# Optimization experiments

Measured on AMD Instinct MI355X. Metric: run time of the kernel, lower is better.

## Reference

```python
import jax, jax.numpy as jnp
import numpy as np

D_MODEL = 1024
NUM_HEADS = 16
HEAD_DIM = D_MODEL // NUM_HEADS
B, S = 2, 2048


def setup_inputs() -> dict:
    key = jax.random.key(0)
    ks = jax.random.split(key, 8)
    scale = 1.0 / np.sqrt(D_MODEL)
    inp = {
        "query": jax.random.normal(ks[0], (B, S, D_MODEL), jnp.float32),
        "key": jax.random.normal(ks[1], (B, S, D_MODEL), jnp.float32),
        "value": jax.random.normal(ks[2], (B, S, D_MODEL), jnp.float32),
        # causal mask, broadcastable over batch and heads
        "mask": jnp.tril(jnp.ones((S, S), dtype=bool))[None, None, :, :],
        # torch nn.Linear weights: y = x @ W.T (+ b)
        "Wq": jax.random.normal(ks[3], (D_MODEL, D_MODEL), jnp.float32) * scale,
        "Wk": jax.random.normal(ks[4], (D_MODEL, D_MODEL), jnp.float32) * scale,
        "Wv": jax.random.normal(ks[5], (D_MODEL, D_MODEL), jnp.float32) * scale,
        "Wo": jax.random.normal(ks[6], (D_MODEL, D_MODEL), jnp.float32) * scale,
        "bo": jax.random.normal(ks[7], (D_MODEL,), jnp.float32) * scale,
    }
    return inp


def _split_heads(x):
    b, s, _ = x.shape
    return x.reshape(b, s, NUM_HEADS, HEAD_DIM).transpose(0, 2, 1, 3)  # [B,H,S,Dh]


def reference(query, key, value, mask, Wq, Wk, Wv, Wo, bo):
    q = _split_heads(query @ Wq.T)
    k = _split_heads(key @ Wk.T)
    v = _split_heads(value @ Wv.T)
    scores = jnp.einsum("bhqd,bhkd->bhqk", q, k) / jnp.sqrt(jnp.float32(HEAD_DIM))
    scores = jnp.where(mask, scores, jnp.float32(-jnp.inf))
    attn = jax.nn.softmax(scores, axis=-1)
    out = jnp.einsum("bhqk,bhkd->bhqd", attn, v)  # [B,H,S,Dh]
    out = out.transpose(0, 2, 1, 3).reshape(query.shape[0], q.shape[2], D_MODEL)
    return out @ Wo.T + bo
```

## Files before the change

kernel.cpp:

```cpp
#include <hip/hip_runtime.h>
#include <hip/hip_bf16.h>

#define DM   1024
#define NH   16
#define HD   64
#define SEQ  2048
#define BATCH 2
#define MTOT (BATCH*SEQ)

typedef unsigned short u16;
typedef __attribute__((ext_vector_type(8))) short bf16x8;
typedef __attribute__((ext_vector_type(4))) float f32x4;

#define SC2F 0.1803368801111464f

__device__ __forceinline__ float bf2f(u16 h) {
  union { unsigned int i; float f; } u; u.i = ((unsigned int)h) << 16; return u.f;
}
__device__ __forceinline__ u16 f2bf(float f) {
  union { float f; unsigned int i; } u; u.f = f;
  unsigned int r = u.i + 0x7fffu + ((u.i >> 16) & 1u);
  return (u16)(r >> 16);
}
__device__ __forceinline__ unsigned int pk2(float lo, float hi) {
  union { float f; unsigned int u; } a, b; a.f = lo; b.f = hi;
  return ((a.u + 0x8000u) >> 16) | ((b.u + 0x8000u) & 0xFFFF0000u);
}
__device__ __forceinline__ unsigned int cvtpk(float lo, float hi) {
  unsigned int r;
  asm("v_cvt_pk_bf16_f32 %0, %1, %2" : "=v"(r) : "v"(lo), "v"(hi));
  return r;
}

__device__ __forceinline__ uint4 load8_bf16(const void* base, size_t elemOff, bool isf32) {
  if (!isf32) return *(const uint4*)((const u16*)base + elemOff);
  const float* f = (const float*)base + elemOff;
  f32x4 a = *(const f32x4*)f;
  f32x4 b = *(const f32x4*)(f + 4);
  union { u16 h[8]; uint4 v; } r;
  r.h[0]=f2bf(a[0]); r.h[1]=f2bf(a[1]); r.h[2]=f2bf(a[2]); r.h[3]=f2bf(a[3]);
  r.h[4]=f2bf(b[0]); r.h[5]=f2bf(b[1]); r.h[6]=f2bf(b[2]); r.h[7]=f2bf(b[3]);
  return r.v;
}

__global__ __launch_bounds__(256) void prep(
    const void* __restrict__ q, const void* __restrict__ k, const void* __restrict__ v,
    const void* __restrict__ wq, const void* __restrict__ wk, const void* __restrict__ wv,
    const void* __restrict__ wo, const void* __restrict__ bo,
    u16* __restrict__ Xq, u16* __restrict__ Xk, u16* __restrict__ Xv,
    u16* __restrict__ Wqb, u16* __restrict__ Wkb, u16* __restrict__ Wvb, u16* __restrict__ Wob,
    float* __restrict__ biasf, int* __restrict__ flag_out)
{
  const int tid = threadIdx.x;
  __shared__ int cnts[4];
  {
    const u16* qs = (const u16*)q;
    int e0 = (qs[tid*2]   >> 7) & 0xFF;
    int e1 = (qs[tid*2+1] >> 7) & 0xFF;
    int c = ((e0 >= 0x6E && e0 <= 0x8F) ? 1 : 0) + ((e1 >= 0x6E && e1 <= 0x8F) ? 1 : 0);
    c += __shfl_xor(c, 1);  c += __shfl_xor(c, 2);  c += __shfl_xor(c, 4);
    c += __shfl_xor(c, 8);  c += __shfl_xor(c, 16); c += __shfl_xor(c, 32);
    if ((tid & 63) == 0) cnts[tid >> 6] = c;
  }
  __syncthreads();
  const bool isf32 = (cnts[0] + cnts[1] + cnts[2] + cnts[3]) < 400;

  const int z = blockIdx.z;
  if (z == 7) {
    if (blockIdx.x == 0) {
      if (tid == 0) *flag_out = isf32 ? 0 : 1;
      for (int i = tid; i < DM; i += 256)
        biasf[i] = isf32 ? ((const float*)bo)[i] : bf2f(((const u16*)bo)[i]);
    }
    return;
  }
  const void* src; u16* dst; size_t n;
  switch (z) {
    case 0: src=q;  dst=Xq;  n=(size_t)MTOT*DM; break;
    case 1: src=k;  dst=Xk;  n=(size_t)MTOT*DM; break;
    case 2: src=v;  dst=Xv;  n=(size_t)MTOT*DM; break;
    case 3: src=wq; dst=Wqb; n=(size_t)DM*DM;   break;
    case 4: src=wk; dst=Wkb; n=(size_t)DM*DM;   break;
    case 5: src=wv; dst=Wvb; n=(size_t)DM*DM;   break;
    default: src=wo; dst=Wob; n=(size_t)DM*DM;  break;
  }
  const size_t stride = (size_t)gridDim.x * 256 * 8;
  for (size_t i = ((size_t)blockIdx.x * 256 + tid) * 8; i < n; i += stride)
    *(uint4*)(dst + i) = load8_bf16(src, i, isf32);
}

__device__ __forceinline__ void gld16(const u16* g, u16* l) {
  __builtin_amdgcn_global_load_lds(
      (const __attribute__((address_space(1))) void*)g,
      (__attribute__((address_space(3))) void*)l, 16, 0, 0);
}

__global__ __launch_bounds__(256) void gemm_qkv(
    const u16* __restrict__ X0, const u16* __restrict__ X1, const u16* __restrict__ X2,
    const u16* __restrict__ W0, const u16* __restrict__ W1, const u16* __restrict__ W2,
    u16* __restrict__ F0, u16* __restrict__ F1, u16* __restrict__ F2)
{
  __shared__ __align__(16) u16 smem[24576];
  u16* const A0 = smem;
  u16* const A1 = smem + 4096;
  u16* const A2 = smem + 8192;
  u16* const B0 = smem + 12288;
  u16* const B1 = smem + 16384;
  u16* const B2 = smem + 20480;

  const int zz = blockIdx.z;
  const u16* X = (zz==0) ? X0 : ((zz==1) ? X1 : X2);
  const u16* W = (zz==0) ? W0 : ((zz==1) ? W1 : W2);
  u16* outF    = (zz==0) ? F0 : ((zz==1) ? F1 : F2);

  const int tid = threadIdx.x;
  const int wave = tid >> 6, lane = tid & 63, quad = lane >> 4, l16 = lane & 15;
  const int wr = wave >> 1, wc = wave & 1;
  const int m0 = blockIdx.x * 128, n0 = blockIdx.y * 128;

  const int sg = ((lane & 3) ^ ((lane >> 3) & 3)) * 8;
  const int rS = wave*32 + (lane >> 2);
  const u16* gA0 = X + (size_t)(m0 + rS)*DM + sg;
  const u16* gA1 = X + (size_t)(m0 + rS + 16)*DM + sg;
  const u16* gB0 = W + (size_t)(n0 + rS)*DM + sg;
  const u16* gB1 = W + (size_t)(n0 + rS + 16)*DM + sg;
  const int so = wave*1024;

  const int xslot8 = (quad ^ ((l16 >> 1) & 3)) * 8;

  f32x4 acc[4][4];
#pragma unroll
  for (int i = 0; i < 4; i++)
#pragma unroll
    for (int j = 0; j < 4; j++) { acc[i][j][0]=0.f; acc[i][j][1]=0.f; acc[i][j][2]=0.f; acc[i][j][3]=0.f; }

  gld16(gA0, A0 + so);
  gld16(gA1, A0 + so + 512);
  gld16(gB0, B0 + so);
  gld16(gB1, B0 + so + 512);
  asm volatile("" ::: "memory");

  int cur = 0;
  for (int k0 = 0; k0 < DM; k0 += 32) {
    u16* const Ab = (cur == 0) ? A0 : ((cur == 1) ? A1 : A2);
    u16* const Bb = (cur == 0) ? B0 : ((cur == 1) ? B1 : B2);
    const int nxt = (cur == 2) ? 0 : cur + 1;
    if (k0 + 32 < DM) {
      u16* const An = (nxt == 0) ? A0 : ((nxt == 1) ? A1 : A2);
      u16* const Bn = (nxt == 0) ? B0 : ((nxt == 1) ? B1 : B2);
      gld16(gA0 + k0 + 32, An + so);
      gld16(gA1 + k0 + 32, An + so + 512);
      gld16(gB0 + k0 + 32, Bn + so);
      gld16(gB1 + k0 + 32, Bn + so + 512);
      asm volatile("s_waitcnt vmcnt(4)" ::: "memory");
    } else {
      asm volatile("s_waitcnt vmcnt(0)" ::: "memory");
    }
    __builtin_amdgcn_s_barrier();
    asm volatile("" ::: "memory");

    bf16x8 af[4], bfr[4];
#pragma unroll
    for (int fr = 0; fr < 4; fr++)
      af[fr] = *(const bf16x8*)&Ab[(wr*64 + fr*16 + l16)*32 + xslot8];
#pragma unroll
    for (int fc = 0; fc < 4; fc++)
      bfr[fc] = *(const bf16x8*)&Bb[(wc*64 + fc*16 + l16)*32 + xslot8];
#pragma unroll
    for (int fr = 0; fr < 4; fr++)
#pragma unroll
      for (int fc = 0; fc < 4; fc++)
        acc[fr][fc] = __builtin_amdgcn_mfma_f32_16x16x32_bf16(af[fr], bfr[fc], acc[fr][fc], 0, 0, 0);

    asm volatile("" ::: "memory");
    cur = nxt;
  }

  if (zz == 2) {
    u16* const Ts = smem;
    const int bb = m0 >> 11;
    const int s0 = m0 & (SEQ-1);
#pragma unroll
    for (int p = 0; p < 2; p++) {
      __syncthreads();
      if (wc == p) {
#pragma unroll
        for (int fr = 0; fr < 4; fr++) {
#pragma unroll
          for (int fc = 0; fc < 4; fc++) {
            const int dl = fc*16 + l16;
            const int sb = wr*64 + fr*16 + quad*4;
            const int slot = (sb >> 3) ^ (dl & 15);
            u16* rowp = &Ts[dl*128 + slot*8 + (sb & 7)];
            *(unsigned int*)(rowp)     = pk2(acc[fr][fc][0], acc[fr][fc][1]);
            *(unsigned int*)(rowp + 2) = pk2(acc[fr][fc][2], acc[fr][fc][3]);
          }
        }
      }
      __syncthreads();
      const int dl2 = tid >> 2, ch4 = tid & 3;
      const int hh = (n0 + p*64) >> 6;
      u16* dst = outF + ((size_t)(bb*NH + hh)*HD + dl2)*SEQ + s0 + ch4*32;
#pragma unroll
      for (int j = 0; j < 4; j++) {
        const int c  = ch4*4 + j;
        const int lo = (c >> 2)*32 + (c & 3)*4;
        const int hi = lo + 16;
        uint2 lo2 = *(const uint2*)&Ts[dl2*128 + (((lo >> 3) ^ (dl2 & 15))*8) + (lo & 7)];
        uint2 hi2 = *(const uint2*)&Ts[dl2*128 + (((hi >> 3) ^ (dl2 & 15))*8) + (hi & 7)];
        uint4 o; o.x = lo2.x; o.y = lo2.y; o.z = hi2.x; o.w = hi2.y;
        *(uint4*)&dst[j*8] = o;
      }
    }
    return;
  }

#pragma unroll
  for (int fr = 0; fr < 4; fr++) {
#pragma unroll
    for (int rr = 0; rr < 4; rr++) {
      const int m = m0 + wr*64 + fr*16 + quad*4 + rr;
#pragma unroll
      for (int fc = 0; fc < 4; fc++) {
        const int n = n0 + wc*64 + fc*16 + l16;
        float vv = acc[fr][fc][rr];
        if (zz == 0) vv *= SC2F;
        const int b = m >> 11, s = m & (SEQ-1), h = n >> 6, d = n & (HD-1);
        outF[((size_t)(b*NH + h)*SEQ + s)*HD + d] = f2bf(vv);
      }
    }
  }
}

__global__ __launch_bounds__(256) void gemm_out(
    const u16* __restrict__ X, const u16* __restrict__ W,
    const float* __restrict__ biasf, void* __restrict__ outP,
    const int* __restrict__ dflag)
{
  __shared__ __align__(16) u16 smem[18432];
  u16* const A0 = smem;
  u16* const A1 = smem + 4096;
  u16* const A2 = smem + 8192;
  u16* const B0 = smem + 12288;
  u16* const B1 = smem + 14336;
  u16* const B2 = smem + 16384;

  const int tid = threadIdx.x;
  const int wave = tid >> 6, lane = tid & 63, quad = lane >> 4, l16 = lane & 15;
  const int wr = wave >> 1, wc = wave & 1;
  const int m0 = blockIdx.x * 128, n0 = blockIdx.y * 64;

  const int sg = ((lane & 3) ^ ((lane >> 3) & 3)) * 8;
  const int rA = wave*32 + (lane >> 2);
  const int rB = wave*16 + (lane >> 2);
  const u16* gA0 = X + (size_t)(m0 + rA)*DM + sg;
  const u16* gA1 = X + (size_t)(m0 + rA + 16)*DM + sg;
  const u16* gB0 = W + (size_t)(n0 + rB)*DM + sg;
  const int soA = wave*1024, soB = wave*512;

  const int xslot8 = (quad ^ ((l16 >> 1) & 3)) * 8;

  f32x4 acc[4][2];
#pragma unroll
  for (int i = 0; i < 4; i++)
#pragma unroll
    for (int j = 0; j < 2; j++) { acc[i][j][0]=0.f; acc[i][j][1]=0.f; acc[i][j][2]=0.f; acc[i][j][3]=0.f; }

  gld16(gA0, A0 + soA);
  gld16(gA1, A0 + soA + 512);
  gld16(gB0, B0 + soB);
  asm volatile("" ::: "memory");

  int cur = 0;
  for (int k0 = 0; k0 < DM; k0 += 32) {
    u16* const Ab = (cur == 0) ? A0 : ((cur == 1) ? A1 : A2);
    u16* const Bb = (cur == 0) ? B0 : ((cur == 1) ? B1 : B2);
    const int nxt = (cur == 2) ? 0 : cur + 1;
    if (k0 + 32 < DM) {
      u16* const An = (nxt == 0) ? A0 : ((nxt == 1) ? A1 : A2);
      u16* const Bn = (nxt == 0) ? B0 : ((nxt == 1) ? B1 : B2);
      gld16(gA0 + k0 + 32, An + soA);
      gld16(gA1 + k0 + 32, An + soA + 512);
      gld16(gB0 + k0 + 32, Bn + soB);
      asm volatile("s_waitcnt vmcnt(3)" ::: "memory");
    } else {
      asm volatile("s_waitcnt vmcnt(0)" ::: "memory");
    }
    __builtin_amdgcn_s_barrier();
    asm volatile("" ::: "memory");

    bf16x8 af[4], bfr[2];
#pragma unroll
    for (int fr = 0; fr < 4; fr++)
      af[fr] = *(const bf16x8*)&Ab[(wr*64 + fr*16 + l16)*32 + xslot8];
#pragma unroll
    for (int fc = 0; fc < 2; fc++)
      bfr[fc] = *(const bf16x8*)&Bb[(wc*32 + fc*16 + l16)*32 + xslot8];
#pragma unroll
    for (int fr = 0; fr < 4; fr++)
#pragma unroll
      for (int fc = 0; fc < 2; fc++)
        acc[fr][fc] = __builtin_amdgcn_mfma_f32_16x16x32_bf16(af[fr], bfr[fc], acc[fr][fc], 0, 0, 0);

    asm volatile("" ::: "memory");
    cur = nxt;
  }

  const bool isf32 = (*dflag == 0);
#pragma unroll
  for (int fr = 0; fr < 4; fr++) {
#pragma unroll
    for (int rr = 0; rr < 4; rr++) {
      const int m = m0 + wr*64 + fr*16 + quad*4 + rr;
#pragma unroll
      for (int fc = 0; fc < 2; fc++) {
        const int n = n0 + wc*32 + fc*16 + l16;
        float vv = acc[fr][fc][rr] + biasf[n];
        if (isf32) ((float*)outP)[(size_t)m*DM + n] = vv;
        else       ((u16*)outP)[(size_t)m*DM + n]   = f2bf(vv);
      }
    }
  }
}

__global__ __launch_bounds__(256) void attn_mfma(
    const u16* __restrict__ Qb, const u16* __restrict__ Kb,
    const u16* __restrict__ Vtb,
    u16* __restrict__ Opart, float* __restrict__ mlpart)
{
  __shared__ u16 Ks[2][64*64];
  __shared__ u16 Vs[2][64*64];

  const int bh = blockIdx.x;
  const int pr = blockIdx.y, z = blockIdx.z;
  const u16* Qp = Qb  + (size_t)bh * SEQ * HD;
  const u16* Kp = Kb  + (size_t)bh * SEQ * HD;
  const u16* Vp = Vtb + (size_t)bh * HD * SEQ;

  const int tid  = threadIdx.x;
  const int wave = tid >> 6, lane = tid & 63, quad = lane >> 4, l16 = lane & 15;

  const int i0 = wave*128 + lane, i1 = i0 + 64;
  const int r0 = i0 >> 3, c0 = (i0 & 7) ^ (r0 & 7);
  const int r1 = i1 >> 3, c1 = (i1 & 7) ^ (r1 & 7);
  const int kq_off0 = r0*HD + c0*8;
  const int kq_off1 = r1*HD + c1*8;
  const int v_off0  = r0*SEQ + c0*8;
  const int v_off1  = r1*SEQ + c1*8;

  const int l7 = l16 & 7;
  const int ql = wave*16 + l16;
  const int so = wave*1024;

  for (int ph = 0; ph < 2; ph++) {
    const int qt = ph ? (31 - pr) : pr;
    const int n = qt + 1, half = (n + 1) >> 1;
    const int klo = z ? half : 0, khi = z ? n : half;
    const int q0 = qt * 64;
    const int qg = q0 + ql;

    const u16* qrow = Qp + (size_t)qg * HD;
    const bf16x8 bq0 = *(const bf16x8*)(qrow + quad*8);
    const bf16x8 bq1 = *(const bf16x8*)(qrow + 32 + quad*8);

    f32x4 O[4];
#pragma unroll
    for (int u = 0; u < 4; u++) { O[u][0]=0.f; O[u][1]=0.f; O[u][2]=0.f; O[u][3]=0.f; }
    float mi = -__builtin_inff();
    f32x4 lv = {0.f, 0.f, 0.f, 0.f};

    if (klo < khi) {
      gld16(Kp + klo*(64*HD) + kq_off0, &Ks[0][so]);
      gld16(Kp + klo*(64*HD) + kq_off1, &Ks[0][so + 512]);
      gld16(Vp + klo*64 + v_off0, &Vs[0][so]);
      gld16(Vp + klo*64 + v_off1, &Vs[0][so + 512]);
    }
    asm volatile("" ::: "memory");

    for (int kt = klo; kt < khi; kt++) {
      const int cb = (kt - klo) & 1;
      const u16* kb = &Ks[cb][0];
      const u16* vb = &Vs[cb][0];
      if (kt + 1 < khi) {
        u16* kn = &Ks[cb ^ 1][so];
        u16* vn = &Vs[cb ^ 1][so];
        gld16(Kp + (kt+1)*(64*HD) + kq_off0, kn);
        gld16(Kp + (kt+1)*(64*HD) + kq_off1, kn + 512);
        gld16(Vp + (kt+1)*64 + v_off0, vn);
        gld16(Vp + (kt+1)*64 + v_off1, vn + 512);
        asm volatile("s_waitcnt vmcnt(4)" ::: "memory");
      } else {
        asm volatile("s_waitcnt vmcnt(0)" ::: "memory");
      }
      __builtin_amdgcn_s_barrier();
      asm volatile("" ::: "memory");

      f32x4 st[4];
#pragma unroll
      for (int t = 0; t < 4; t++) { st[t][0]=0.f; st[t][1]=0.f; st[t][2]=0.f; st[t][3]=0.f; }
#pragma unroll
      for (int s = 0; s < 2; s++) {
        const bf16x8 bq = s ? bq1 : bq0;
        const int ch = s*4 + quad;
#pragma unroll
        for (int t = 0; t < 4; t++) {
          bf16x8 ak = *(const bf16x8*)&kb[((t*16 + l16)*8 + (ch ^ l7))*8];
          st[t] = __builtin_amdgcn_mfma_f32_16x16x32_bf16(ak, bq, st[t], 0, 0, 0);
        }
      }

      if (kt == qt) {
#pragma unroll
        for (int t = 0; t < 4; t++)
#pragma unroll
          for (int r = 0; r < 4; r++)
            if (kt*64 + t*16 + quad*4 + r > qg) st[t][r] = -__builtin_inff();
      }

      f32x4 m01 = __builtin_elementwise_max(st[0], st[1]);
      f32x4 m23 = __builtin_elementwise_max(st[2], st[3]);
      f32x4 mm  = __builtin_elementwise_max(m01, m23);
      float mx = fmaxf(fmaxf(mm[0], mm[1]), fmaxf(mm[2], mm[3]));
      mx = fmaxf(mx, __shfl_xor(mx, 16));
      mx = fmaxf(mx, __shfl_xor(mx, 32));

      if (__any(mx > mi + 8.0f)) {
        const float nm = fmaxf(mi, mx);
        const float al = exp2f(mi - nm);
        mi = nm;
        const f32x4 alv = {al, al, al, al};
        lv *= alv;
        O[0] *= alv; O[1] *= alv; O[2] *= alv; O[3] *= alv;
      }

      const f32x4 miv = {mi, mi, mi, mi};
      unsigned int w[4][2];
      f32x4 e0, e1, e2, e3;
      {
        f32x4 d0 = st[0] - miv, d1 = st[1] - miv, d2 = st[2] - miv, d3 = st[3] - miv;
        e0[0]=exp2f(d0[0]); e0[1]=exp2f(d0[1]); e0[2]=exp2f(d0[2]); e0[3]=exp2f(d0[3]);
        e1[0]=exp2f(d1[0]); e1[1]=exp2f(d1[1]); e1[2]=exp2f(d1[2]); e1[3]=exp2f(d1[3]);
        e2[0]=exp2f(d2[0]); e2[1]=exp2f(d2[1]); e2[2]=exp2f(d2[2]); e2[3]=exp2f(d2[3]);
        e3[0]=exp2f(d3[0]); e3[1]=exp2f(d3[1]); e3[2]=exp2f(d3[2]); e3[3]=exp2f(d3[3]);
      }
      w[0][0] = cvtpk(e0[0], e0[1]); w[0][1] = cvtpk(e0[2], e0[3]);
      w[1][0] = cvtpk(e1[0], e1[1]); w[1][1] = cvtpk(e1[2], e1[3]);
      w[2][0] = cvtpk(e2[0], e2[1]); w[2][1] = cvtpk(e2[2], e2[3]);
      w[3][0] = cvtpk(e3[0], e3[1]); w[3][1] = cvtpk(e3[2], e3[3]);
      lv += (e0 + e1) + (e2 + e3);

#pragma unroll
      for (int s = 0; s < 2; s++) {
        union { unsigned int u[4]; bf16x8 v; } bp;
        bp.u[0] = w[2*s][0];   bp.u[1] = w[2*s][1];
        bp.u[2] = w[2*s+1][0]; bp.u[3] = w[2*s+1][1];
        const int ch = s*4 + quad;
#pragma unroll
        for (int u = 0; u < 4; u++) {
          bf16x8 av = *(const bf16x8*)&vb[((u*16 + l16)*8 + (ch ^ l7))*8];
          O[u] = __builtin_amdgcn_mfma_f32_16x16x32_bf16(av, bp.v, O[u], 0, 0, 0);
        }
      }

      asm volatile("" ::: "memory");
      __builtin_amdgcn_s_barrier();
      asm volatile("" ::: "memory");
    }

    float ls = (lv[0] + lv[1]) + (lv[2] + lv[3]);
    ls += __shfl_xor(ls, 16);
    ls += __shfl_xor(ls, 32);

    const int pi = (bh*32 + qt)*2 + z;
    u16* op = Opart + (size_t)pi*4096 + ql*64;
#pragma unroll
    for (int u = 0; u < 4; u++) {
      uint2 u2; u2.x = pk2(O[u][0], O[u][1]); u2.y = pk2(O[u][2], O[u][3]);
      *(uint2*)&op[u*16 + quad*4] = u2;
    }
    if (quad == 0) {
      float2 ml2; ml2.x = mi; ml2.y = ls;
      *(float2*)&mlpart[(size_t)pi*128 + ql*2] = ml2;
    }
  }
}

__global__ __launch_bounds__(64) void attn_merge(
    const u16* __restrict__ Opart, const float* __restrict__ mlpart,
    u16* __restrict__ aO)
{
  const int g = blockIdx.x;
  const int bh = g & 31, qt = g >> 5;
  const int b = bh >> 4, h = bh & 15;
  const int t = threadIdx.x;
  const int pi0 = (bh*32 + qt)*2, pi1 = pi0 + 1;

  const float2 ml0 = *(const float2*)&mlpart[(size_t)pi0*128 + t*2];
  const float2 ml1 = *(const float2*)&mlpart[(size_t)pi1*128 + t*2];
  const float M = fmaxf(ml0.x, ml1.x);
  float w0 = exp2f(ml0.x - M), w1 = exp2f(ml1.x - M);
  const float inv = 1.0f / (w0*ml0.y + w1*ml1.y);
  w0 *= inv; w1 *= inv;

  const u16* o0 = Opart + (size_t)pi0*4096 + t*64;
  const u16* o1 = Opart + (size_t)pi1*4096 + t*64;
  u16* out = aO + (size_t)(b*SEQ + qt*64 + t)*DM + h*HD;
#pragma unroll
  for (int d0 = 0; d0 < 64; d0 += 8) {
    union { uint4 v; u16 h[8]; } a, c; union { uint4 v; u16 h[8]; } bb;
    a.v  = *(const uint4*)&o0[d0];
    bb.v = *(const uint4*)&o1[d0];
#pragma unroll
    for (int j = 0; j < 8; j += 2) {
      float x0 = w0*bf2f(a.h[j])   + w1*bf2f(bb.h[j]);
      float x1 = w0*bf2f(a.h[j+1]) + w1*bf2f(bb.h[j+1]);
      unsigned int pk = pk2(x0, x1);
      c.h[j] = (u16)(pk & 0xFFFF); c.h[j+1] = (u16)(pk >> 16);
    }
    *(uint4*)&out[d0] = c.v;
  }
}

extern "C" void kernel_launch(void* const* d_in, const int* in_sizes, int n_in,
                              void* d_out, int out_size, void* d_ws, size_t ws_size,
                              hipStream_t stream) {
  const void* q  = d_in[0];
  const void* k  = d_in[1];
  const void* v  = d_in[2];
  const void* wq = d_in[4];
  const void* wk = d_in[5];
  const void* wv = d_in[6];
  const void* wo = d_in[7];
  const void* bo = d_in[8];

  const size_t TX = (size_t)MTOT*DM;
  const size_t TW = (size_t)DM*DM;
  u16* ws  = (u16*)d_ws;
  u16* Xq  = ws;
  u16* Xk  = ws + TX;
  u16* Xv  = ws + 2*TX;
  u16* Wqb = ws + 3*TX;
  u16* Wkb = Wqb + TW;
  u16* Wvb = Wqb + 2*TW;
  u16* Wob = Wqb + 3*TW;
  u16* Qw  = ws + 3*TX + 4*TW;
  u16* Kw  = Qw + TX;
  u16* Vt  = Qw + 2*TX;
  u16*   Opart  = Xk;
  float* mlpart = (float*)Wqb;
  u16*   aO     = Xq;
  float* biasf  = (float*)(Qw + 3*TX);
  int*   fl     = (int*)(biasf + DM);

  dim3 blk(256);
  prep<<<dim3(512, 1, 8), blk, 0, stream>>>(q, k, v, wq, wk, wv, wo, bo,
      Xq, Xk, Xv, Wqb, Wkb, Wvb, Wob, biasf, fl);
  gemm_qkv<<<dim3(MTOT/128, DM/128, 3), blk, 0, stream>>>(
      Xq, Xk, Xv, Wqb, Wkb, Wvb, Qw, Kw, Vt);
  attn_mfma<<<dim3(BATCH*NH, 16, 2), blk, 0, stream>>>(Qw, Kw, Vt, Opart, mlpart);
  attn_merge<<<dim3(32*32), dim3(64), 0, stream>>>(Opart, mlpart, aO);
  gemm_out<<<dim3(MTOT/128, DM/64), blk, 0, stream>>>(aO, Wob, biasf, d_out, fl);
}
```

Baseline: 230.3 us.

## Drop split-K attention and merge kernel; one block per query tile

Replaces the split-KV attention (two partial halves per query tile plus a separate merge kernel) with one block per query tile that walks the full causal key range and normalizes its output directly. Query tiles are mapped to blocks in an interleaved long/short order to balance causal work. This removes the merge launch and the round trip of partial outputs and statistics through global memory. In exchange each block is serial over up to 32 key tiles with only 1024 blocks, so load imbalance and the critical path may grow.

```diff
diff --git a/kernel.cpp b/kernel.cpp
--- a/kernel.cpp
+++ b/kernel.cpp
@@ -326,13 +326,19 @@
 __global__ __launch_bounds__(256) void attn_mfma(
     const u16* __restrict__ Qb, const u16* __restrict__ Kb,
     const u16* __restrict__ Vtb,
-    u16* __restrict__ Opart, float* __restrict__ mlpart)
+    u16* __restrict__ aO)
 {
   __shared__ u16 Ks[2][64*64];
   __shared__ u16 Vs[2][64*64];
 
   const int bh = blockIdx.x;
-  const int pr = blockIdx.y, z = blockIdx.z;
+  const int py = blockIdx.y;
+  int qt;
+  if      (py < 8)  qt = 31 - py;
+  else if (py < 16) qt = py - 8;
+  else if (py < 24) qt = 39 - py;
+  else              qt = py - 16;
+
   const u16* Qp = Qb  + (size_t)bh * SEQ * HD;
   const u16* Kp = Kb  + (size_t)bh * SEQ * HD;
   const u16* Vp = Vtb + (size_t)bh * HD * SEQ;
@@ -352,172 +358,128 @@
   const int ql = wave*16 + l16;
   const int so = wave*1024;
 
-  for (int ph = 0; ph < 2; ph++) {
-    const int qt = ph ? (31 - pr) : pr;
-    const int n = qt + 1, half = (n + 1) >> 1;
-    const int klo = z ? half : 0, khi = z ? n : half;
-    const int q0 = qt * 64;
-    const int qg = q0 + ql;
-
-    const u16* qrow = Qp + (size_t)qg * HD;
-    const bf16x8 bq0 = *(const bf16x8*)(qrow + quad*8);
-    const bf16x8 bq1 = *(const bf16x8*)(qrow + 32 + quad*8);
-
-    f32x4 O[4];
-#pragma unroll
-    for (int u = 0; u < 4; u++) { O[u][0]=0.f; O[u][1]=0.f; O[u][2]=0.f; O[u][3]=0.f; }
-    float mi = -__builtin_inff();
-    f32x4 lv = {0.f, 0.f, 0.f, 0.f};
-
-    if (klo < khi) {
-      gld16(Kp + klo*(64*HD) + kq_off0, &Ks[0][so]);
-      gld16(Kp + klo*(64*HD) + kq_off1, &Ks[0][so + 512]);
-      gld16(Vp + klo*64 + v_off0, &Vs[0][so]);
-      gld16(Vp + klo*64 + v_off1, &Vs[0][so + 512]);
-    }
-    asm volatile("" ::: "memory");
-
-    for (int kt = klo; kt < khi; kt++) {
-      const int cb = (kt - klo) & 1;
-      const u16* kb = &Ks[cb][0];
-      const u16* vb = &Vs[cb][0];
-      if (kt + 1 < khi) {
-        u16* kn = &Ks[cb ^ 1][so];
-        u16* vn = &Vs[cb ^ 1][so];
-        gld16(Kp + (kt+1)*(64*HD) + kq_off0, kn);
-        gld16(Kp + (kt+1)*(64*HD) + kq_off1, kn + 512);
-        gld16(Vp + (kt+1)*64 + v_off0, vn);
-        gld16(Vp + (kt+1)*64 + v_off1, vn + 512);
-        asm volatile("s_waitcnt vmcnt(4)" ::: "memory");
-      } else {
-        asm volatile("s_waitcnt vmcnt(0)" ::: "memory");
+  const int khi = qt + 1;
+  const int qg = qt*64 + ql;
+
+  const u16* qrow = Qp + (size_t)qg * HD;
+  const bf16x8 bq0 = *(const bf16x8*)(qrow + quad*8);
+  const bf16x8 bq1 = *(const bf16x8*)(qrow + 32 + quad*8);
+
+  f32x4 O[4];
+#pragma unroll
+  for (int u = 0; u < 4; u++) { O[u][0]=0.f; O[u][1]=0.f; O[u][2]=0.f; O[u][3]=0.f; }
+  float mi = -__builtin_inff();
+  f32x4 lv = {0.f, 0.f, 0.f, 0.f};
+
+  gld16(Kp + kq_off0, &Ks[0][so]);
+  gld16(Kp + kq_off1, &Ks[0][so + 512]);
+  gld16(Vp + v_off0, &Vs[0][so]);
+  gld16(Vp + v_off1, &Vs[0][so + 512]);
+  asm volatile("" ::: "memory");
+
+  for (int kt = 0; kt < khi; kt++) {
+    const int cb = kt & 1;
+    const u16* kb = &Ks[cb][0];
+    const u16* vb = &Vs[cb][0];
+    if (kt + 1 < khi) {
+      u16* kn = &Ks[cb ^ 1][so];
+      u16* vn = &Vs[cb ^ 1][so];
+      gld16(Kp + (kt+1)*(64*HD) + kq_off0, kn);
+      gld16(Kp + (kt+1)*(64*HD) + kq_off1, kn + 512);
+      gld16(Vp + (kt+1)*64 + v_off0, vn);
+      gld16(Vp + (kt+1)*64 + v_off1, vn + 512);
+      asm volatile("s_waitcnt vmcnt(4)" ::: "memory");
+    } else {
+      asm volatile("s_waitcnt vmcnt(0)" ::: "memory");
+    }
+    __builtin_amdgcn_s_barrier();
+    asm volatile("" ::: "memory");
+
+    f32x4 st[4];
+#pragma unroll
+    for (int t = 0; t < 4; t++) { st[t][0]=0.f; st[t][1]=0.f; st[t][2]=0.f; st[t][3]=0.f; }
+#pragma unroll
+    for (int s = 0; s < 2; s++) {
+      const bf16x8 bq = s ? bq1 : bq0;
+      const int ch = s*4 + quad;
+#pragma unroll
+      for (int t = 0; t < 4; t++) {
+        bf16x8 ak = *(const bf16x8*)&kb[((t*16 + l16)*8 + (ch ^ l7))*8];
+        st[t] = __builtin_amdgcn_mfma_f32_16x16x32_bf16(ak, bq, st[t], 0, 0, 0);
       }
-      __builtin_amdgcn_s_barrier();
-      asm volatile("" ::: "memory");
-
-      f32x4 st[4];
-#pragma unroll
-      for (int t = 0; t < 4; t++) { st[t][0]=0.f; st[t][1]=0.f; st[t][2]=0.f; st[t][3]=0.f; }
-#pragma unroll
-      for (int s = 0; s < 2; s++) {
-        const bf16x8 bq = s ? bq1 : bq0;
-        const int ch = s*4 + quad;
-#pragma unroll
-        for (int t = 0; t < 4; t++) {
-          bf16x8 ak = *(const bf16x8*)&kb[((t*16 + l16)*8 + (ch ^ l7))*8];
-          st[t] = __builtin_amdgcn_mfma_f32_16x16x32_bf16(ak, bq, st[t], 0, 0, 0);
-        }
+    }
+
+    if (kt == qt) {
+#pragma unroll
+      for (int t = 0; t < 4; t++)
+#pragma unroll
+        for (int r = 0; r < 4; r++)
+          if (kt*64 + t*16 + quad*4 + r > qg) st[t][r] = -__builtin_inff();
+    }
+
+    f32x4 m01 = __builtin_elementwise_max(st[0], st[1]);
+    f32x4 m23 = __builtin_elementwise_max(st[2], st[3]);
+    f32x4 mm  = __builtin_elementwise_max(m01, m23);
+    float mx = fmaxf(fmaxf(mm[0], mm[1]), fmaxf(mm[2], mm[3]));
+    mx = fmaxf(mx, __shfl_xor(mx, 16));
+    mx = fmaxf(mx, __shfl_xor(mx, 32));
+
+    if (__any(mx > mi + 8.0f)) {
+      const float nm = fmaxf(mi, mx);
+      const float al = exp2f(mi - nm);
+      mi = nm;
+      const f32x4 alv = {al, al, al, al};
+      lv *= alv;
+      O[0] *= alv; O[1] *= alv; O[2] *= alv; O[3] *= alv;
+    }
+
+    const f32x4 miv = {mi, mi, mi, mi};
+    unsigned int w[4][2];
+    f32x4 e0, e1, e2, e3;
+    {
+      f32x4 d0 = st[0] - miv, d1 = st[1] - miv, d2 = st[2] - miv, d3 = st[3] - miv;
+      e0[0]=exp2f(d0[0]); e0[1]=exp2f(d0[1]); e0[2]=exp2f(d0[2]); e0[3]=exp2f(d0[3]);
+      e1[0]=exp2f(d1[0]); e1[1]=exp2f(d1[1]); e1[2]=exp2f(d1[2]); e1[3]=exp2f(d1[3]);
+      e2[0]=exp2f(d2[0]); e2[1]=exp2f(d2[1]); e2[2]=exp2f(d2[2]); e2[3]=exp2f(d2[3]);
+      e3[0]=exp2f(d3[0]); e3[1]=exp2f(d3[1]); e3[2]=exp2f(d3[2]); e3[3]=exp2f(d3[3]);
+    }
+    w[0][0] = cvtpk(e0[0], e0[1]); w[0][1] = cvtpk(e0[2], e0[3]);
+    w[1][0] = cvtpk(e1[0], e1[1]); w[1][1] = cvtpk(e1[2], e1[3]);
+    w[2][0] = cvtpk(e2[0], e2[1]); w[2][1] = cvtpk(e2[2], e2[3]);
+    w[3][0] = cvtpk(e3[0], e3[1]); w[3][1] = cvtpk(e3[2], e3[3]);
+    lv += (e0 + e1) + (e2 + e3);
+
+#pragma unroll
+    for (int s = 0; s < 2; s++) {
+      union { unsigned int u[4]; bf16x8 v; } bp;
+      bp.u[0] = w[2*s][0];   bp.u[1] = w[2*s][1];
+      bp.u[2] = w[2*s+1][0]; bp.u[3] = w[2*s+1][1];
+      const int ch = s*4 + quad;
+#pragma unroll
+      for (int u = 0; u < 4; u++) {
+        bf16x8 av = *(const bf16x8*)&vb[((u*16 + l16)*8 + (ch ^ l7))*8];
+        O[u] = __builtin_amdgcn_mfma_f32_16x16x32_bf16(av, bp.v, O[u], 0, 0, 0);
       }
-
-      if (kt == qt) {
-#pragma unroll
-        for (int t = 0; t < 4; t++)
-#pragma unroll
-          for (int r = 0; r < 4; r++)
-            if (kt*64 + t*16 + quad*4 + r > qg) st[t][r] = -__builtin_inff();
-      }
-
-      f32x4 m01 = __builtin_elementwise_max(st[0], st[1]);
-      f32x4 m23 = __builtin_elementwise_max(st[2], st[3]);
-      f32x4 mm  = __builtin_elementwise_max(m01, m23);
-      float mx = fmaxf(fmaxf(mm[0], mm[1]), fmaxf(mm[2], mm[3]));
-      mx = fmaxf(mx, __shfl_xor(mx, 16));
-      mx = fmaxf(mx, __shfl_xor(mx, 32));
-
-      if (__any(mx > mi + 8.0f)) {
-        const float nm = fmaxf(mi, mx);
-        const float al = exp2f(mi - nm);
-        mi = nm;
-        const f32x4 alv = {al, al, al, al};
-        lv *= alv;
-        O[0] *= alv; O[1] *= alv; O[2] *= alv; O[3] *= alv;
-      }
-
-      const f32x4 miv = {mi, mi, mi, mi};
-      unsigned int w[4][2];
-      f32x4 e0, e1, e2, e3;
-      {
-        f32x4 d0 = st[0] - miv, d1 = st[1] - miv, d2 = st[2] - miv, d3 = st[3] - miv;
-        e0[0]=exp2f(d0[0]); e0[1]=exp2f(d0[1]); e0[2]=exp2f(d0[2]); e0[3]=exp2f(d0[3]);
-        e1[0]=exp2f(d1[0]); e1[1]=exp2f(d1[1]); e1[2]=exp2f(d1[2]); e1[3]=exp2f(d1[3]);
-        e2[0]=exp2f(d2[0]); e2[1]=exp2f(d2[1]); e2[2]=exp2f(d2[2]); e2[3]=exp2f(d2[3]);
-        e3[0]=exp2f(d3[0]); e3[1]=exp2f(d3[1]); e3[2]=exp2f(d3[2]); e3[3]=exp2f(d3[3]);
-      }
-      w[0][0] = cvtpk(e0[0], e0[1]); w[0][1] = cvtpk(e0[2], e0[3]);
-      w[1][0] = cvtpk(e1[0], e1[1]); w[1][1] = cvtpk(e1[2], e1[3]);
-      w[2][0] = cvtpk(e2[0], e2[1]); w[2][1] = cvtpk(e2[2], e2[3]);
-      w[3][0] = cvtpk(e3[0], e3[1]); w[3][1] = cvtpk(e3[2], e3[3]);
-      lv += (e0 + e1) + (e2 + e3);
-
-#pragma unroll
-      for (int s = 0; s < 2; s++) {
-        union { unsigned int u[4]; bf16x8 v; } bp;
-        bp.u[0] = w[2*s][0];   bp.u[1] = w[2*s][1];
-        bp.u[2] = w[2*s+1][0]; bp.u[3] = w[2*s+1][1];
-        const int ch = s*4 + quad;
-#pragma unroll
-        for (int u = 0; u < 4; u++) {
-          bf16x8 av = *(const bf16x8*)&vb[((u*16 + l16)*8 + (ch ^ l7))*8];
-          O[u] = __builtin_amdgcn_mfma_f32_16x16x32_bf16(av, bp.v, O[u], 0, 0, 0);
-        }
-      }
-
-      asm volatile("" ::: "memory");
-      __builtin_amdgcn_s_barrier();
-      asm volatile("" ::: "memory");
-    }
-
-    float ls = (lv[0] + lv[1]) + (lv[2] + lv[3]);
-    ls += __shfl_xor(ls, 16);
-    ls += __shfl_xor(ls, 32);
-
-    const int pi = (bh*32 + qt)*2 + z;
-    u16* op = Opart + (size_t)pi*4096 + ql*64;
-#pragma unroll
-    for (int u = 0; u < 4; u++) {
-      uint2 u2; u2.x = pk2(O[u][0], O[u][1]); u2.y = pk2(O[u][2], O[u][3]);
-      *(uint2*)&op[u*16 + quad*4] = u2;
-    }
-    if (quad == 0) {
-      float2 ml2; ml2.x = mi; ml2.y = ls;
-      *(float2*)&mlpart[(size_t)pi*128 + ql*2] = ml2;
-    }
-  }
-}
-
-__global__ __launch_bounds__(64) void attn_merge(
-    const u16* __restrict__ Opart, const float* __restrict__ mlpart,
-    u16* __restrict__ aO)
-{
-  const int g = blockIdx.x;
-  const int bh = g & 31, qt = g >> 5;
+    }
+
+    asm volatile("" ::: "memory");
+    __builtin_amdgcn_s_barrier();
+    asm volatile("" ::: "memory");
+  }
+
+  float ls = (lv[0] + lv[1]) + (lv[2] + lv[3]);
+  ls += __shfl_xor(ls, 16);
+  ls += __shfl_xor(ls, 32);
+  const float inv = 1.0f / ls;
+
   const int b = bh >> 4, h = bh & 15;
-  const int t = threadIdx.x;
-  const int pi0 = (bh*32 + qt)*2, pi1 = pi0 + 1;
-
-  const float2 ml0 = *(const float2*)&mlpart[(size_t)pi0*128 + t*2];
-  const float2 ml1 = *(const float2*)&mlpart[(size_t)pi1*128 + t*2];
-  const float M = fmaxf(ml0.x, ml1.x);
-  float w0 = exp2f(ml0.x - M), w1 = exp2f(ml1.x - M);
-  const float inv = 1.0f / (w0*ml0.y + w1*ml1.y);
-  w0 *= inv; w1 *= inv;
-
-  const u16* o0 = Opart + (size_t)pi0*4096 + t*64;
-  const u16* o1 = Opart + (size_t)pi1*4096 + t*64;
-  u16* out = aO + (size_t)(b*SEQ + qt*64 + t)*DM + h*HD;
-#pragma unroll
-  for (int d0 = 0; d0 < 64; d0 += 8) {
-    union { uint4 v; u16 h[8]; } a, c; union { uint4 v; u16 h[8]; } bb;
-    a.v  = *(const uint4*)&o0[d0];
-    bb.v = *(const uint4*)&o1[d0];
-#pragma unroll
-    for (int j = 0; j < 8; j += 2) {
-      float x0 = w0*bf2f(a.h[j])   + w1*bf2f(bb.h[j]);
-      float x1 = w0*bf2f(a.h[j+1]) + w1*bf2f(bb.h[j+1]);
-      unsigned int pk = pk2(x0, x1);
-      c.h[j] = (u16)(pk & 0xFFFF); c.h[j+1] = (u16)(pk >> 16);
-    }
-    *(uint4*)&out[d0] = c.v;
+  u16* outp = aO + ((size_t)(b*SEQ + qt*64 + ql))*DM + h*HD;
+#pragma unroll
+  for (int u = 0; u < 4; u++) {
+    uint2 u2;
+    u2.x = pk2(O[u][0]*inv, O[u][1]*inv);
+    u2.y = pk2(O[u][2]*inv, O[u][3]*inv);
+    *(uint2*)&outp[u*16 + quad*4] = u2;
   }
 }
 
@@ -546,8 +508,6 @@
   u16* Qw  = ws + 3*TX + 4*TW;
   u16* Kw  = Qw + TX;
   u16* Vt  = Qw + 2*TX;
-  u16*   Opart  = Xk;
-  float* mlpart = (float*)Wqb;
   u16*   aO     = Xq;
   float* biasf  = (float*)(Qw + 3*TX);
   int*   fl     = (int*)(biasf + DM);
@@ -557,7 +517,6 @@
       Xq, Xk, Xv, Wqb, Wkb, Wvb, Wob, biasf, fl);
   gemm_qkv<<<dim3(MTOT/128, DM/128, 3), blk, 0, stream>>>(
       Xq, Xk, Xv, Wqb, Wkb, Wvb, Qw, Kw, Vt);
-  attn_mfma<<<dim3(BATCH*NH, 16, 2), blk, 0, stream>>>(Qw, Kw, Vt, Opart, mlpart);
-  attn_merge<<<dim3(32*32), dim3(64), 0, stream>>>(Opart, mlpart, aO);
+  attn_mfma<<<dim3(BATCH*NH, 32, 1), blk, 0, stream>>>(Qw, Kw, Vt, aO);
   gemm_out<<<dim3(MTOT/128, DM/64), blk, 0, stream>>>(aO, Wob, biasf, d_out, fl);
 }
```

Result: faster. 224.9 us, median of 2 (-2.3%).
